# Kernel optimization log

Measured on AMD Instinct MI355X. Metric: run time of the kernel, lower is better.

Reference implementation:

```python
import jax, jax.numpy as jnp
import numpy as np

B, S, H, V = 4, 512, 256, 32000


def setup_inputs() -> dict:
    key = jax.random.key(0)
    ks = jax.random.split(key, 6)
    s = 0.02
    x = jax.random.randint(ks[0], (B, S), 0, V)
    emb = jax.random.normal(ks[1], (V, H), dtype=jnp.float32) * s
    W_ih = jax.random.normal(ks[2], (3 * H, H), dtype=jnp.float32) * s
    W_hh = jax.random.normal(ks[3], (3 * H, H), dtype=jnp.float32) * s
    b_ih = jnp.zeros((3 * H,), jnp.float32)
    b_hh = jnp.zeros((3 * H,), jnp.float32)
    W_out = jax.random.normal(ks[4], (V, H), dtype=jnp.float32) * s
    b_out = jnp.zeros((V,), jnp.float32)
    return dict(x=x, emb=emb, W_ih=W_ih, W_hh=W_hh, b_ih=b_ih, b_hh=b_hh,
                W_out=W_out, b_out=b_out)


def gru_sequence(embedded, W_ih, W_hh, b_ih, b_hh):
    # embedded: [B, S, H]; precompute all input projections once: [B, S, 3H]
    xp = jnp.einsum('bsh,gh->bsg', embedded, W_ih) + b_ih
    Hdim = W_hh.shape[1]
    h0 = jnp.zeros((embedded.shape[0], Hdim), embedded.dtype)

    def step(h, xt):  # xt: [B, 3H]
        hp = h @ W_hh.T + b_hh  # [B, 3H]
        xr, xz, xn = jnp.split(xt, 3, axis=-1)
        hr, hz, hn = jnp.split(hp, 3, axis=-1)
        r = jax.nn.sigmoid(xr + hr)
        z = jax.nn.sigmoid(xz + hz)
        n = jnp.tanh(xn + r * hn)
        h_new = (1.0 - z) * n + z * h
        return h_new, h_new

    _, hs = jax.lax.scan(step, h0, jnp.swapaxes(xp, 0, 1))  # [S, B, H]
    return jnp.swapaxes(hs, 0, 1)  # [B, S, H]


def reference(x, emb, W_ih, W_hh, b_ih, b_hh, W_out, b_out):
    embedded = emb[x]                                   # [B, S, H]
    rnn_out = gru_sequence(embedded, W_ih, W_hh, b_ih, b_hh)
    logits = jnp.einsum('bsh,vh->bsv', rnn_out, W_out) + b_out  # [B, S, V]
    # symbolic constraint: if prev token == 0, tokens >= 3 are invalid (t > 0)
    prev_zero = (x[:, :-1] == 0)                        # [B, S-1]
    prev_zero = jnp.pad(prev_zero, ((0, 0), (1, 0)))    # t=0 never masked
    vocab_ge3 = jnp.arange(logits.shape[-1]) >= 3       # [V]
    invalid = prev_zero[:, :, None] & vocab_ge3[None, None, :]
    return jnp.where(invalid, -jnp.inf, logits)
```

## Files before the change

### kernel.cpp

```cpp
#include <hip/hip_runtime.h>
#include <hip/hip_bf16.h>

typedef __attribute__((ext_vector_type(8))) short bf16x8;
typedef __attribute__((ext_vector_type(4))) float f32x4;
typedef __attribute__((ext_vector_type(4))) unsigned short u16x4;

#define HB 256
#define G3 768
#define SQ 512
#define NBATCH 4
#define NV 32000

__device__ __forceinline__ unsigned short f2bf(float f) {
    unsigned int u = __float_as_uint(f);
    u = u + 0x7FFFu + ((u >> 16) & 1u);
    return (unsigned short)(u >> 16);
}

__global__ void k_prep(const float* __restrict__ W_ih, const float* __restrict__ W_hh,
                       const float* __restrict__ W_out, float* __restrict__ w_ihT,
                       unsigned short* __restrict__ wfrag, unsigned short* __restrict__ woutbf,
                       int do_wout) {
    int stride = gridDim.x * blockDim.x;
    int tid = blockIdx.x * blockDim.x + threadIdx.x;
    for (int e = tid; e < G3 * HB; e += stride) {
        int k = e / G3, g = e - k * G3;
        w_ihT[e] = W_ih[g * HB + k];
    }
    for (int e = tid; e < G3 * HB; e += stride) {
        int i = e & 7, l = (e >> 3) & 63, c = (e >> 9) & 7, s = (e >> 12) & 3;
        int q = e >> 14;
        int g = q % 3, w = q / 3;
        int row = g * 256 + 64 * w + 16 * s + (l & 15);
        int kk = 32 * c + 8 * (l >> 4) + i;
        wfrag[e] = f2bf(W_hh[row * HB + kk]);
    }
    if (do_wout) {
        for (int e = tid; e < NV * HB; e += stride) woutbf[e] = f2bf(W_out[e]);
    }
}

__global__ __launch_bounds__(256) void k_embed_xp(
        const int* __restrict__ x, const float* __restrict__ emb,
        const float* __restrict__ w_ihT, const float* __restrict__ b_ih,
        const float* __restrict__ b_hh, float* __restrict__ xp) {
    __shared__ float e[8][HB];
    int tid = threadIdx.x;
    int tok0 = blockIdx.x * 8;
    {
        int s = tid >> 5, k0 = (tid & 31) * 8;
        long idx = x[tok0 + s];
        const float* src = emb + idx * (long)HB + k0;
        f32x4 a = *(const f32x4*)src, bq = *(const f32x4*)(src + 4);
        *(f32x4*)&e[s][k0] = a;
        *(f32x4*)&e[s][k0 + 4] = bq;
    }
    __syncthreads();
    #pragma unroll
    for (int it = 0; it < 3; ++it) {
        int gg = tid + it * 256;
        float acc[8] = {0.f, 0.f, 0.f, 0.f, 0.f, 0.f, 0.f, 0.f};
        for (int k = 0; k < HB; k += 4) {
            float w0 = w_ihT[(k + 0) * G3 + gg];
            float w1 = w_ihT[(k + 1) * G3 + gg];
            float w2 = w_ihT[(k + 2) * G3 + gg];
            float w3 = w_ihT[(k + 3) * G3 + gg];
            #pragma unroll
            for (int s = 0; s < 8; ++s) {
                f32x4 ev = *(const f32x4*)&e[s][k];
                acc[s] += w0 * ev.x + w1 * ev.y + w2 * ev.z + w3 * ev.w;
            }
        }
        float bias = b_ih[gg] + (gg < 512 ? b_hh[gg] : 0.f);
        #pragma unroll
        for (int s = 0; s < 8; ++s)
            xp[(size_t)(tok0 + s) * G3 + gg] = acc[s] + bias;
    }
}

__global__ __attribute__((amdgpu_waves_per_eu(1, 1))) __launch_bounds__(256)
void k_gru(const float* __restrict__ xp, const unsigned short* __restrict__ wfrag,
           const float* __restrict__ b_hh, unsigned short* __restrict__ rnn) {
    __shared__ unsigned short hbf[2][NBATCH][HB];

    int tid = threadIdx.x;
    int w = tid >> 6, l = tid & 63;
    int c15 = l & 15, hi = l >> 4;
    int b4 = c15 & 3;
    int g4 = c15 >> 2;
    int swz = (b4 & 1) << 6;

    bf16x8 Arz[2][4][8];
    bf16x8 An[4][8];
    #pragma unroll
    for (int g = 0; g < 2; ++g)
        #pragma unroll
        for (int s = 0; s < 4; ++s)
            #pragma unroll
            for (int c = 0; c < 8; ++c) {
                Arz[g][s][c] = ((const bf16x8*)wfrag)[(((w * 3 + g) * 4 + s) * 8 + c) * 64 + l];
                asm volatile("" : "+a"(Arz[g][s][c]));
            }
    #pragma unroll
    for (int s = 0; s < 4; ++s)
        #pragma unroll
        for (int c = 0; c < 8; ++c) {
            An[s][c] = ((const bf16x8*)wfrag)[(((w * 3 + 2) * 4 + s) * 8 + c) * 64 + l];
            asm volatile("" : "+v"(An[s][c]));
        }

    for (int k = tid; k < 2 * NBATCH * HB; k += 256) ((unsigned short*)hbf)[k] = 0;

    int iL = 64 * w + 16 * g4 + 4 * hi;
    f32x4 bnv = *(const f32x4*)&b_hh[512 + iL];
    f32x4 H = {0.f, 0.f, 0.f, 0.f};
    const f32x4 zz = {0.f, 0.f, 0.f, 0.f};

    const float* xpb = xp + (size_t)b4 * SQ * G3 + iL;
    unsigned short* rnb = rnn + (size_t)b4 * SQ * HB + iL;
    __syncthreads();

    for (int t = 0; t < SQ; ++t) {
        int cur = t & 1, nxt = cur ^ 1;
        const char* hbb = (const char*)hbf + cur * 2048 + b4 * 512;

        f32x4 xr = *(const f32x4*)(xpb);
        f32x4 xz = *(const f32x4*)(xpb + 256);
        f32x4 xn = *(const f32x4*)(xpb + 512);

        f32x4 ar[4], az[4], an[4];
        #pragma unroll
        for (int s = 0; s < 4; ++s) { ar[s] = zz; az[s] = zz; an[s] = zz; }

        bf16x8 BfA = *(const bf16x8*)(hbb + ((16 * hi) ^ swz));
        #pragma unroll
        for (int c = 0; c < 8; ++c) {
            bf16x8 BfN;
            if (c < 7)
                BfN = *(const bf16x8*)(hbb + ((64 * (c + 1) + 16 * hi) ^ swz));
            #pragma unroll
            for (int s = 0; s < 4; ++s) {
                asm("v_mfma_f32_16x16x32_bf16 %0, %1, %2, %0"
                    : "+v"(ar[s]) : "a"(Arz[0][s][c]), "v"(BfA));
                asm("v_mfma_f32_16x16x32_bf16 %0, %1, %2, %0"
                    : "+v"(az[s]) : "a"(Arz[1][s][c]), "v"(BfA));
                an[s] = __builtin_amdgcn_mfma_f32_16x16x32_bf16(An[s][c], BfA, an[s], 0, 0, 0);
            }
            if (c < 7) BfA = BfN;
        }
        asm volatile("s_nop 7\n\ts_nop 7"
                     : "+v"(ar[0]), "+v"(ar[1]), "+v"(ar[2]), "+v"(ar[3]),
                       "+v"(az[0]), "+v"(az[1]), "+v"(az[2]), "+v"(az[3]));

        bool s1 = (g4 & 1) != 0, s2 = (g4 & 2) != 0;
        f32x4 sAr = s2 ? (s1 ? ar[3] : ar[2]) : (s1 ? ar[1] : ar[0]);
        f32x4 sAz = s2 ? (s1 ? az[3] : az[2]) : (s1 ? az[1] : az[0]);
        f32x4 sAn = s2 ? (s1 ? an[3] : an[2]) : (s1 ? an[1] : an[0]);

        u16x4 pack;
        #pragma unroll
        for (int j = 0; j < 4; ++j) {
            float r = __builtin_amdgcn_rcpf(1.f + __expf(-(xr[j] + sAr[j])));
            float z = __builtin_amdgcn_rcpf(1.f + __expf(-(xz[j] + sAz[j])));
            float narg = xn[j] + r * (sAn[j] + bnv[j]);
            float n = 1.f - 2.f * __builtin_amdgcn_rcpf(__expf(2.f * narg) + 1.f);
            float hv = (1.f - z) * n + z * H[j];
            H[j] = hv;
            pack[j] = f2bf(hv);
        }
        *(u16x4*)((char*)hbf + nxt * 2048 + b4 * 512 + ((iL * 2) ^ swz)) = pack;
        *(u16x4*)rnb = pack;

        __syncthreads();
        xpb += G3;
        rnb += HB;
    }
}

template <int CONV>
__global__ __launch_bounds__(256) void k_logits(
        const unsigned short* __restrict__ rnn, const unsigned short* __restrict__ woutbf,
        const float* __restrict__ woutf, const float* __restrict__ b_out,
        const int* __restrict__ x, float* __restrict__ out) {
    int tid = threadIdx.x;
    int wv = tid >> 6, l = tid & 63;
    int wm = wv >> 1, wn = wv & 1;
    int c15 = l & 15, hi = l >> 4;
    int m0 = blockIdx.y * 128 + wm * 64;
    int n0 = blockIdx.x * 128 + wn * 64;

    const f32x4 zz = {0.f, 0.f, 0.f, 0.f};
    f32x4 acc[4][4];
    #pragma unroll
    for (int i = 0; i < 4; ++i)
        #pragma unroll
        for (int j = 0; j < 4; ++j) acc[i][j] = zz;

    #pragma unroll
    for (int c = 0; c < 8; ++c) {
        bf16x8 af[4], bfr[4];
        #pragma unroll
        for (int rt = 0; rt < 4; ++rt)
            af[rt] = *(const bf16x8*)(rnn + (size_t)(m0 + rt * 16 + c15) * HB + 32 * c + 8 * hi);
        #pragma unroll
        for (int ct = 0; ct < 4; ++ct) {
            if (CONV) {
                const float* s = woutf + (size_t)(n0 + ct * 16 + c15) * HB + 32 * c + 8 * hi;
                f32x4 lo = *(const f32x4*)s, hi4 = *(const f32x4*)(s + 4);
                bf16x8 bb;
                #pragma unroll
                for (int q = 0; q < 4; ++q) bb[q] = (short)f2bf(lo[q]);
                #pragma unroll
                for (int q = 0; q < 4; ++q) bb[4 + q] = (short)f2bf(hi4[q]);
                bfr[ct] = bb;
            } else {
                bfr[ct] = *(const bf16x8*)(woutbf + (size_t)(n0 + ct * 16 + c15) * HB + 32 * c + 8 * hi);
            }
        }
        #pragma unroll
        for (int rt = 0; rt < 4; ++rt)
            #pragma unroll
            for (int ct = 0; ct < 4; ++ct)
                acc[rt][ct] = __builtin_amdgcn_mfma_f32_16x16x32_bf16(af[rt], bfr[ct], acc[rt][ct], 0, 0, 0);
    }

    float bo[4];
    #pragma unroll
    for (int ct = 0; ct < 4; ++ct) bo[ct] = b_out[n0 + ct * 16 + c15];

    const float NEGINF = -__builtin_inff();
    #pragma unroll
    for (int rt = 0; rt < 4; ++rt) {
        #pragma unroll
        for (int j = 0; j < 4; ++j) {
            int m = m0 + rt * 16 + 4 * hi + j;
            int tt = m & (SQ - 1);
            bool bad = (tt > 0) && (x[m - 1] == 0);
            float* orow = out + (size_t)m * NV;
            #pragma unroll
            for (int ct = 0; ct < 4; ++ct) {
                int v = n0 + ct * 16 + c15;
                float val = acc[rt][ct][j] + bo[ct];
                if (bad && v >= 3) val = NEGINF;
                orow[v] = val;
            }
        }
    }
}

extern "C" void kernel_launch(void* const* d_in, const int* in_sizes, int n_in,
                              void* d_out, int out_size, void* d_ws, size_t ws_size,
                              hipStream_t stream) {
    const int*   x     = (const int*)d_in[0];
    const float* emb   = (const float*)d_in[1];
    const float* W_ih  = (const float*)d_in[2];
    const float* W_hh  = (const float*)d_in[3];
    const float* b_ih  = (const float*)d_in[4];
    const float* b_hh  = (const float*)d_in[5];
    const float* W_out = (const float*)d_in[6];
    const float* b_out = (const float*)d_in[7];
    float* out = (float*)d_out;

    char* ws = (char*)d_ws;
    float*          xp     = (float*)(ws);
    float*          w_ihT  = (float*)(ws + 6291456);
    unsigned short* wfrag  = (unsigned short*)(ws + 7077888);
    unsigned short* rnn    = (unsigned short*)(ws + 7471104);
    unsigned short* woutbf = (unsigned short*)(ws + 8519680);
    int use_woutbf = (ws_size >= (size_t)24903680) ? 1 : 0;

    k_prep<<<2048, 256, 0, stream>>>(W_ih, W_hh, W_out, w_ihT, wfrag, woutbf, use_woutbf);
    k_embed_xp<<<256, 256, 0, stream>>>(x, emb, w_ihT, b_ih, b_hh, xp);
    k_gru<<<1, 256, 0, stream>>>(xp, wfrag, b_hh, rnn);
    dim3 g3(NV / 128, 2048 / 128);
    if (use_woutbf)
        k_logits<0><<<g3, 256, 0, stream>>>(rnn, woutbf, nullptr, b_out, x, out);
    else
        k_logits<1><<<g3, 256, 0, stream>>>(rnn, nullptr, W_out, b_out, x, out);
}
```

Measured before the change: 810.4 us.

## Split GRU step MFMAs per gate and overlap gate math with matmuls

```diff
diff --git a/kernel.cpp b/kernel.cpp
--- a/kernel.cpp
+++ b/kernel.cpp
@@ -3,6 +3,7 @@
 
 typedef __attribute__((ext_vector_type(8))) short bf16x8;
 typedef __attribute__((ext_vector_type(4))) float f32x4;
+typedef __attribute__((ext_vector_type(2))) unsigned int u32x2;
 typedef __attribute__((ext_vector_type(4))) unsigned short u16x4;
 
 #define HB 256
@@ -115,63 +116,107 @@
     f32x4 bnv = *(const f32x4*)&b_hh[512 + iL];
     f32x4 H = {0.f, 0.f, 0.f, 0.f};
     const f32x4 zz = {0.f, 0.f, 0.f, 0.f};
+    bool s1 = (g4 & 1) != 0, s2 = (g4 & 2) != 0;
 
     const float* xpb = xp + (size_t)b4 * SQ * G3 + iL;
     unsigned short* rnb = rnn + (size_t)b4 * SQ * HB + iL;
+    const char* hbbase = (const char*)hbf + b4 * 512;
+    char* wrb = (char*)hbf + b4 * 512 + ((iL * 2) ^ swz);
     __syncthreads();
 
     for (int t = 0; t < SQ; ++t) {
-        int cur = t & 1, nxt = cur ^ 1;
-        const char* hbb = (const char*)hbf + cur * 2048 + b4 * 512;
+        int cur = (t & 1) << 11, nxt = cur ^ 2048;
 
         f32x4 xr = *(const f32x4*)(xpb);
+        f32x4 a0 = zz, a1 = zz, a2 = zz, a3 = zz;
+        {
+            bf16x8 BfA = *(const bf16x8*)(hbbase + cur + ((16 * hi) ^ swz));
+            #pragma unroll
+            for (int c = 0; c < 8; ++c) {
+                bf16x8 BfN;
+                if (c < 7)
+                    BfN = *(const bf16x8*)(hbbase + cur + ((64 * (c + 1) + 16 * hi) ^ swz));
+                asm("v_mfma_f32_16x16x32_bf16 %0, %1, %2, %0" : "+v"(a0) : "a"(Arz[0][0][c]), "v"(BfA));
+                asm("v_mfma_f32_16x16x32_bf16 %0, %1, %2, %0" : "+v"(a1) : "a"(Arz[0][1][c]), "v"(BfA));
+                asm("v_mfma_f32_16x16x32_bf16 %0, %1, %2, %0" : "+v"(a2) : "a"(Arz[0][2][c]), "v"(BfA));
+                asm("v_mfma_f32_16x16x32_bf16 %0, %1, %2, %0" : "+v"(a3) : "a"(Arz[0][3][c]), "v"(BfA));
+                if (c < 7) BfA = BfN;
+            }
+        }
+
         f32x4 xz = *(const f32x4*)(xpb + 256);
+        f32x4 z0 = zz, z1 = zz, z2 = zz, z3 = zz;
+        {
+            bf16x8 BfA = *(const bf16x8*)(hbbase + cur + ((16 * hi) ^ swz));
+            #pragma unroll
+            for (int c = 0; c < 8; ++c) {
+                bf16x8 BfN;
+                if (c < 7)
+                    BfN = *(const bf16x8*)(hbbase + cur + ((64 * (c + 1) + 16 * hi) ^ swz));
+                asm("v_mfma_f32_16x16x32_bf16 %0, %1, %2, %0" : "+v"(z0) : "a"(Arz[1][0][c]), "v"(BfA));
+                asm("v_mfma_f32_16x16x32_bf16 %0, %1, %2, %0" : "+v"(z1) : "a"(Arz[1][1][c]), "v"(BfA));
+                asm("v_mfma_f32_16x16x32_bf16 %0, %1, %2, %0" : "+v"(z2) : "a"(Arz[1][2][c]), "v"(BfA));
+                asm("v_mfma_f32_16x16x32_bf16 %0, %1, %2, %0" : "+v"(z3) : "a"(Arz[1][3][c]), "v"(BfA));
+                if (c < 7) BfA = BfN;
+            }
+        }
+
+        asm("s_nop 7\n\ts_nop 7" : "+v"(a0), "+v"(a1), "+v"(a2), "+v"(a3));
+        f32x4 vr_lo = s1 ? a1 : a0, vr_hi = s1 ? a3 : a2;
+        f32x4 vr = s2 ? vr_hi : vr_lo;
+        float rr0 = __builtin_amdgcn_rcpf(1.f + __expf(-(xr.x + vr.x)));
+        float rr1 = __builtin_amdgcn_rcpf(1.f + __expf(-(xr.y + vr.y)));
+        float rr2 = __builtin_amdgcn_rcpf(1.f + __expf(-(xr.z + vr.z)));
+        float rr3 = __builtin_amdgcn_rcpf(1.f + __expf(-(xr.w + vr.w)));
+
         f32x4 xn = *(const f32x4*)(xpb + 512);
-
-        f32x4 ar[4], az[4], an[4];
-        #pragma unroll
-        for (int s = 0; s < 4; ++s) { ar[s] = zz; az[s] = zz; an[s] = zz; }
-
-        bf16x8 BfA = *(const bf16x8*)(hbb + ((16 * hi) ^ swz));
-        #pragma unroll
-        for (int c = 0; c < 8; ++c) {
-            bf16x8 BfN;
-            if (c < 7)
-                BfN = *(const bf16x8*)(hbb + ((64 * (c + 1) + 16 * hi) ^ swz));
-            #pragma unroll
-            for (int s = 0; s < 4; ++s) {
-                asm("v_mfma_f32_16x16x32_bf16 %0, %1, %2, %0"
-                    : "+v"(ar[s]) : "a"(Arz[0][s][c]), "v"(BfA));
-                asm("v_mfma_f32_16x16x32_bf16 %0, %1, %2, %0"
-                    : "+v"(az[s]) : "a"(Arz[1][s][c]), "v"(BfA));
-                an[s] = __builtin_amdgcn_mfma_f32_16x16x32_bf16(An[s][c], BfA, an[s], 0, 0, 0);
-            }
-            if (c < 7) BfA = BfN;
-        }
-        asm volatile("s_nop 7\n\ts_nop 7"
-                     : "+v"(ar[0]), "+v"(ar[1]), "+v"(ar[2]), "+v"(ar[3]),
-                       "+v"(az[0]), "+v"(az[1]), "+v"(az[2]), "+v"(az[3]));
-
-        bool s1 = (g4 & 1) != 0, s2 = (g4 & 2) != 0;
-        f32x4 sAr = s2 ? (s1 ? ar[3] : ar[2]) : (s1 ? ar[1] : ar[0]);
-        f32x4 sAz = s2 ? (s1 ? az[3] : az[2]) : (s1 ? az[1] : az[0]);
-        f32x4 sAn = s2 ? (s1 ? an[3] : an[2]) : (s1 ? an[1] : an[0]);
-
-        u16x4 pack;
-        #pragma unroll
-        for (int j = 0; j < 4; ++j) {
-            float r = __builtin_amdgcn_rcpf(1.f + __expf(-(xr[j] + sAr[j])));
-            float z = __builtin_amdgcn_rcpf(1.f + __expf(-(xz[j] + sAz[j])));
-            float narg = xn[j] + r * (sAn[j] + bnv[j]);
-            float n = 1.f - 2.f * __builtin_amdgcn_rcpf(__expf(2.f * narg) + 1.f);
-            float hv = (1.f - z) * n + z * H[j];
-            H[j] = hv;
-            pack[j] = f2bf(hv);
-        }
-        *(u16x4*)((char*)hbf + nxt * 2048 + b4 * 512 + ((iL * 2) ^ swz)) = pack;
-        *(u16x4*)rnb = pack;
-
-        __syncthreads();
+        f32x4 n0a = zz, n1a = zz, n2a = zz, n3a = zz;
+        {
+            bf16x8 BfA = *(const bf16x8*)(hbbase + cur + ((16 * hi) ^ swz));
+            #pragma unroll
+            for (int c = 0; c < 8; ++c) {
+                bf16x8 BfN;
+                if (c < 7)
+                    BfN = *(const bf16x8*)(hbbase + cur + ((64 * (c + 1) + 16 * hi) ^ swz));
+                n0a = __builtin_amdgcn_mfma_f32_16x16x32_bf16(An[0][c], BfA, n0a, 0, 0, 0);
+                n1a = __builtin_amdgcn_mfma_f32_16x16x32_bf16(An[1][c], BfA, n1a, 0, 0, 0);
+                n2a = __builtin_amdgcn_mfma_f32_16x16x32_bf16(An[2][c], BfA, n2a, 0, 0, 0);
+                n3a = __builtin_amdgcn_mfma_f32_16x16x32_bf16(An[3][c], BfA, n3a, 0, 0, 0);
+                if (c < 7) BfA = BfN;
+            }
+        }
+
+        asm("s_nop 7\n\ts_nop 7" : "+v"(z0), "+v"(z1), "+v"(z2), "+v"(z3));
+        f32x4 vz_lo = s1 ? z1 : z0, vz_hi = s1 ? z3 : z2;
+        f32x4 vz = s2 ? vz_hi : vz_lo;
+        float zg0 = __builtin_amdgcn_rcpf(1.f + __expf(-(xz.x + vz.x)));
+        float zg1 = __builtin_amdgcn_rcpf(1.f + __expf(-(xz.y + vz.y)));
+        float zg2 = __builtin_amdgcn_rcpf(1.f + __expf(-(xz.z + vz.z)));
+        float zg3 = __builtin_amdgcn_rcpf(1.f + __expf(-(xz.w + vz.w)));
+
+        f32x4 vn_lo = s1 ? n1a : n0a, vn_hi = s1 ? n3a : n2a;
+        f32x4 vn = s2 ? vn_hi : vn_lo;
+        float ng0 = 1.f - 2.f * __builtin_amdgcn_rcpf(__expf(2.f * (xn.x + rr0 * (vn.x + bnv.x))) + 1.f);
+        float ng1 = 1.f - 2.f * __builtin_amdgcn_rcpf(__expf(2.f * (xn.y + rr1 * (vn.y + bnv.y))) + 1.f);
+        float ng2 = 1.f - 2.f * __builtin_amdgcn_rcpf(__expf(2.f * (xn.z + rr2 * (vn.z + bnv.z))) + 1.f);
+        float ng3 = 1.f - 2.f * __builtin_amdgcn_rcpf(__expf(2.f * (xn.w + rr3 * (vn.w + bnv.w))) + 1.f);
+        float h0 = (1.f - zg0) * ng0 + zg0 * H.x;
+        float h1 = (1.f - zg1) * ng1 + zg1 * H.y;
+        float h2 = (1.f - zg2) * ng2 + zg2 * H.z;
+        float h3 = (1.f - zg3) * ng3 + zg3 * H.w;
+        H.x = h0; H.y = h1; H.z = h2; H.w = h3;
+
+        unsigned int p0, p1;
+        asm("v_cvt_pk_bf16_f32 %0, %1, %2" : "=v"(p0) : "v"(h0), "v"(h1));
+        asm("v_cvt_pk_bf16_f32 %0, %1, %2" : "=v"(p1) : "v"(h2), "v"(h3));
+        u32x2 pk = {p0, p1};
+        *(u32x2*)(wrb + nxt) = pk;
+        *(u32x2*)rnb = pk;
+
+        asm volatile("s_waitcnt lgkmcnt(0)" ::: "memory");
+        __builtin_amdgcn_sched_barrier(0);
+        __builtin_amdgcn_s_barrier();
+
         xpb += G3;
         rnb += HB;
     }
@@ -209,9 +254,9 @@
                 f32x4 lo = *(const f32x4*)s, hi4 = *(const f32x4*)(s + 4);
                 bf16x8 bb;
                 #pragma unroll
-                for (int q = 0; q < 4; ++q) bb[q] = (short)f2bf(lo[q]);
+                for (int qq = 0; qq < 4; ++qq) bb[qq] = (short)f2bf(lo[qq]);
                 #pragma unroll
-                for (int q = 0; q < 4; ++q) bb[4 + q] = (short)f2bf(hi4[q]);
+                for (int qq = 0; qq < 4; ++qq) bb[4 + qq] = (short)f2bf(hi4[qq]);
                 bfr[ct] = bb;
             } else {
                 bfr[ct] = *(const bf16x8*)(woutbf + (size_t)(n0 + ct * 16 + c15) * HB + 32 * c + 8 * hi);
```

Measured after the change: 851.6 us. +5.1%, slower.
